# Optimization experiments

Measured on AMD Instinct MI355X. Metric: run time of the kernel, lower is better.

Reference implementation:

```python
import jax, jax.numpy as jnp
import numpy as np
from jax import lax

K_ITERS = 35

def _conv3x3_same(x, w, b):
    # x: [B,1,H,W], w: [1,1,3,3]
    y = lax.conv_general_dilated(x, w, window_strides=(1, 1),
                                 padding=((1, 1), (1, 1)),
                                 dimension_numbers=('NCHW', 'OIHW', 'NCHW'))
    return y + b.reshape(1, -1, 1, 1)

def _maxpool3x3_same(v):
    # 3x3 max pool, stride 1, padding 1 (torch MaxPool2d(kernel=3, stride=1, padding=1))
    return lax.reduce_window(v, -jnp.inf, lax.max,
                             window_dimensions=(1, 1, 3, 3),
                             window_strides=(1, 1, 1, 1),
                             padding=((0, 0), (0, 0), (1, 1), (1, 1)))

def setup_inputs() -> dict:
    key = jax.random.key(0)
    k1, k2, k3 = jax.random.split(key, 3)
    B, H, W = 64, 192, 192
    X = jax.random.uniform(k1, (B, 2, H, W), dtype=jnp.float32)  # grid, goal in [0,1)
    hp_w = jax.random.uniform(k2, (1, 1, 3, 3), dtype=jnp.float32) * 0.5
    p_w = jax.random.uniform(k3, (1, 1, 3, 3), dtype=jnp.float32) * 0.5
    hp_b = jnp.zeros((1,), dtype=jnp.float32)
    p_b = jnp.zeros((1,), dtype=jnp.float32)
    return {"X": X, "hp_w": hp_w, "hp_b": hp_b, "p_w": p_w, "p_b": p_b}

def reference(X, hp_w, hp_b, p_w, p_b):
    grid = X[:, 0:1]           # [B,1,H,W]
    goal = X[:, 1:2]           # [B,1,H,W]
    r = -(1.0 - goal)          # reward map in [-1, 0]
    # process_image: double conv -> wall/flow probability p in (0,1)
    h = jax.nn.relu(_conv3x3_same(grid, hp_w, hp_b))
    p = jax.nn.sigmoid(_conv3x3_same(h, p_w, p_b))
    # value iteration: v = max(v, r + p * (maxpool(v) - r)), k=35 steps
    def body(_, v):
        return jnp.maximum(v, r + p * (_maxpool3x3_same(v) - r))
    v = lax.fori_loop(0, K_ITERS, body, r)
    return (v[:, 0], p[:, 0])  # squeeze channel dim -> ([B,H,W], [B,H,W])
```

## Files before the change

kernel.cpp:

```cpp
#include <hip/hip_runtime.h>

#define HH 192
#define WW 192
#define HW 36864
#define BB 64
#define NPIX 2359296
#define NEG (-1.0e30f)

__global__ __launch_bounds__(256) void k_conv_fused(const float* __restrict__ X,
                                                    const float* __restrict__ hw9,
                                                    const float* __restrict__ hb,
                                                    const float* __restrict__ pw9,
                                                    const float* __restrict__ pb,
                                                    float* __restrict__ p_out) {
  int idx = blockIdx.x * 256 + threadIdx.x;
  if (idx >= NPIX / 4) return;
  int b = idx / (HW / 4);
  int rem = idx - b * (HW / 4);
  int y = rem / 48;
  int ch = rem - y * 48;
  int x0 = ch * 4;
  const float* g = X + (size_t)b * (2 * HW);

  float gr[5][8];
#pragma unroll
  for (int ry = 0; ry < 5; ++ry) {
    int yy = y - 2 + ry;
    if (yy < 0 || yy >= HH) {
#pragma unroll
      for (int j = 0; j < 8; ++j) gr[ry][j] = 0.f;
    } else {
      const float* row = g + yy * WW;
      float4 a = (x0 >= 4) ? *(const float4*)(row + x0 - 4) : make_float4(0, 0, 0, 0);
      float4 m = *(const float4*)(row + x0);
      float4 cq = (x0 + 4 < WW) ? *(const float4*)(row + x0 + 4) : make_float4(0, 0, 0, 0);
      gr[ry][0] = a.z; gr[ry][1] = a.w;
      gr[ry][2] = m.x; gr[ry][3] = m.y; gr[ry][4] = m.z; gr[ry][5] = m.w;
      gr[ry][6] = cq.x; gr[ry][7] = cq.y;
    }
  }
  float hwv[9], pwv[9];
#pragma unroll
  for (int i = 0; i < 9; ++i) { hwv[i] = hw9[i]; pwv[i] = pw9[i]; }
  float hbv = hb[0], pbv = pb[0];

  float hr[3][6];
#pragma unroll
  for (int ry = 0; ry < 3; ++ry) {
    int yy = y - 1 + ry;
    bool rowok = (yy >= 0 && yy < HH);
#pragma unroll
    for (int j = 0; j < 6; ++j) {
      int xx = x0 - 1 + j;
      float acc = hbv;
#pragma unroll
      for (int di = 0; di < 3; ++di)
#pragma unroll
        for (int dj = 0; dj < 3; ++dj)
          acc = fmaf(gr[ry + di][j + dj], hwv[di * 3 + dj], acc);
      hr[ry][j] = (rowok && xx >= 0 && xx < WW) ? fmaxf(acc, 0.f) : 0.f;
    }
  }
  float o[4];
#pragma unroll
  for (int k = 0; k < 4; ++k) {
    float acc = pbv;
#pragma unroll
    for (int di = 0; di < 3; ++di)
#pragma unroll
      for (int dj = 0; dj < 3; ++dj)
        acc = fmaf(hr[di][k + dj], pwv[di * 3 + dj], acc);
    o[k] = 1.f / (1.f + __expf(-acc));
  }
  *(float4*)(p_out + (size_t)b * HW + y * WW + x0) = make_float4(o[0], o[1], o[2], o[3]);
}

template <int FIRST>
__global__ __launch_bounds__(256, 1) void k_span(const float* __restrict__ v_in,
                                                 const float* __restrict__ p_glob,
                                                 const float* __restrict__ X,
                                                 float* __restrict__ v_out) {
  int wid = blockIdx.x * 4 + (threadIdx.x >> 6);
  int lane = threadIdx.x & 63;
  int b = wid >> 4;
  int t = wid & 15;
  int ti = t >> 2, tj = t & 3;
  int ly = lane >> 3, lx = lane & 7;
  int py = ti * 48 - 8 + ly * 8;
  int px = tj * 48 - 8 + lx * 8;
  bool colok = (px >= 0 && px < WW);

  const float* gimg = X + (size_t)b * (2 * HW) + HW;
  const float* pimg = p_glob + (size_t)b * HW;
  const float* vimg = v_in + (size_t)b * HW;

  float v[8][8], p[8][8], c[8][8];

#pragma unroll
  for (int r = 0; r < 8; ++r) {
    int gy = py + r;
    if (colok && gy >= 0 && gy < HH) {
      *(float4*)&p[r][0] = *(const float4*)(pimg + gy * WW + px);
      *(float4*)&p[r][4] = *(const float4*)(pimg + gy * WW + px + 4);
    }
  }
#pragma unroll
  for (int r = 0; r < 8; ++r) {
    int gy = py + r;
    if (colok && gy >= 0 && gy < HH) {
      *(float4*)&c[r][0] = *(const float4*)(gimg + gy * WW + px);
      *(float4*)&c[r][4] = *(const float4*)(gimg + gy * WW + px + 4);
    }
  }
  if (!FIRST) {
#pragma unroll
    for (int r = 0; r < 8; ++r) {
      int gy = py + r;
      if (colok && gy >= 0 && gy < HH) {
        *(float4*)&v[r][0] = *(const float4*)(vimg + gy * WW + px);
        *(float4*)&v[r][4] = *(const float4*)(vimg + gy * WW + px + 4);
      }
    }
  }

#pragma unroll
  for (int r = 0; r < 8; ++r) {
    int gy = py + r;
    if (colok && gy >= 0 && gy < HH) {
#pragma unroll
      for (int j = 0; j < 8; ++j) {
        float gg = c[r][j];
        if (FIRST) v[r][j] = gg - 1.f;
        c[r][j] = (gg - 1.f) * (1.f - p[r][j]);
      }
    } else {
#pragma unroll
      for (int j = 0; j < 8; ++j) { v[r][j] = NEG; p[r][j] = 0.f; c[r][j] = NEG; }
    }
  }

  int lup = (lane - 8) & 63, ldn = (lane + 8) & 63;
  int llt = (lane - 1) & 63, lrt = (lane + 1) & 63;

#pragma unroll 1
  for (int it = 0; it < 7; ++it) {
    float th[8], bh[8];
#pragma unroll
    for (int j = 0; j < 8; ++j) { float s = __shfl(v[7][j], lup, 64); th[j] = (ly == 0) ? NEG : s; }
#pragma unroll
    for (int j = 0; j < 8; ++j) { float s = __shfl(v[0][j], ldn, 64); bh[j] = (ly == 7) ? NEG : s; }
    float vm[8][8];
#pragma unroll
    for (int r = 0; r < 8; ++r) {
#pragma unroll
      for (int j = 0; j < 8; ++j) {
        float up = (r == 0) ? th[j] : v[r - 1][j];
        float dn = (r == 7) ? bh[j] : v[r + 1][j];
        vm[r][j] = fmaxf(fmaxf(up, dn), v[r][j]);
      }
    }
#pragma unroll
    for (int r = 0; r < 8; ++r) {
      float sl = __shfl(vm[r][7], llt, 64);
      float sr = __shfl(vm[r][0], lrt, 64);
      float lvm = (lx == 0) ? NEG : sl;
      float rvm = (lx == 7) ? NEG : sr;
      float hm0 = fmaxf(lvm, fmaxf(vm[r][0], vm[r][1]));
      float hm7 = fmaxf(vm[r][6], fmaxf(vm[r][7], rvm));
      v[r][0] = fmaxf(v[r][0], fmaf(p[r][0], hm0, c[r][0]));
#pragma unroll
      for (int j = 1; j < 7; ++j) {
        float hm = fmaxf(vm[r][j - 1], fmaxf(vm[r][j], vm[r][j + 1]));
        v[r][j] = fmaxf(v[r][j], fmaf(p[r][j], hm, c[r][j]));
      }
      v[r][7] = fmaxf(v[r][7], fmaf(p[r][7], hm7, c[r][7]));
    }
  }

  if (ly >= 1 && ly <= 6 && lx >= 1 && lx <= 6) {
    float* wimg = v_out + (size_t)b * HW;
#pragma unroll
    for (int r = 0; r < 8; ++r) {
      *(float4*)(wimg + (py + r) * WW + px) = make_float4(v[r][0], v[r][1], v[r][2], v[r][3]);
      *(float4*)(wimg + (py + r) * WW + px + 4) = make_float4(v[r][4], v[r][5], v[r][6], v[r][7]);
    }
  }
}

extern "C" void kernel_launch(void* const* d_in, const int* in_sizes, int n_in,
                              void* d_out, int out_size, void* d_ws, size_t ws_size,
                              hipStream_t stream) {
  const float* X = (const float*)d_in[0];
  const float* hp_w = (const float*)d_in[1];
  const float* hp_b = (const float*)d_in[2];
  const float* p_w = (const float*)d_in[3];
  const float* p_b = (const float*)d_in[4];

  float* out = (float*)d_out;
  float* out_v = out;
  float* out_p = out + NPIX;
  float* bufA = (float*)d_ws;

  int nblk = (NPIX / 4 + 255) / 256;
  k_conv_fused<<<nblk, 256, 0, stream>>>(X, hp_w, hp_b, p_w, p_b, out_p);

  k_span<1><<<256, 256, 0, stream>>>(X , out_p, X, out_v);
  k_span<0><<<256, 256, 0, stream>>>(out_v, out_p, X, bufA);
  k_span<0><<<256, 256, 0, stream>>>(bufA, out_p, X, out_v);
  k_span<0><<<256, 256, 0, stream>>>(out_v, out_p, X, bufA);
  k_span<0><<<256, 256, 0, stream>>>(bufA, out_p, X, out_v);
}
```

Before: 160.8 us.

## Fuse five value-iteration span kernels into one cooperative kernel with grid sync

Replaces the five separate span launches with a single cooperative kernel. It keeps p, c and v in registers across spans and uses grid.sync between spans, so only the halo lanes reload v from global memory after each span. This is meant to remove four launch gaps and the repeated global loads of p, goal and v. In exchange it adds grid barrier cost and needs a second workspace buffer, and it falls back to the old launches if the cooperative launch fails.

```diff
diff --git a/kernel.cpp b/kernel.cpp
--- a/kernel.cpp
+++ b/kernel.cpp
@@ -1,9 +1,10 @@
 #include <hip/hip_runtime.h>
+#include <hip/hip_cooperative_groups.h>
+namespace cg = cooperative_groups;
 
 #define HH 192
 #define WW 192
 #define HW 36864
-#define BB 64
 #define NPIX 2359296
 #define NEG (-1.0e30f)
 
@@ -75,6 +76,129 @@
   *(float4*)(p_out + (size_t)b * HW + y * WW + x0) = make_float4(o[0], o[1], o[2], o[3]);
 }
 
+__device__ __forceinline__ void iter7(float v[8][8], const float p[8][8], const float c[8][8],
+                                      int ly, int lx, int lup, int ldn, int llt, int lrt) {
+#pragma unroll 1
+  for (int it = 0; it < 7; ++it) {
+    float th[8], bh[8];
+#pragma unroll
+    for (int j = 0; j < 8; ++j) { float s = __shfl(v[7][j], lup, 64); th[j] = (ly == 0) ? NEG : s; }
+#pragma unroll
+    for (int j = 0; j < 8; ++j) { float s = __shfl(v[0][j], ldn, 64); bh[j] = (ly == 7) ? NEG : s; }
+    float vm[8][8];
+#pragma unroll
+    for (int r = 0; r < 8; ++r) {
+#pragma unroll
+      for (int j = 0; j < 8; ++j) {
+        float up = (r == 0) ? th[j] : v[r - 1][j];
+        float dn = (r == 7) ? bh[j] : v[r + 1][j];
+        vm[r][j] = fmaxf(fmaxf(up, dn), v[r][j]);
+      }
+    }
+#pragma unroll
+    for (int r = 0; r < 8; ++r) {
+      float sl = __shfl(vm[r][7], llt, 64);
+      float sr = __shfl(vm[r][0], lrt, 64);
+      float lvm = (lx == 0) ? NEG : sl;
+      float rvm = (lx == 7) ? NEG : sr;
+      float hm0 = fmaxf(lvm, fmaxf(vm[r][0], vm[r][1]));
+      float hm7 = fmaxf(vm[r][6], fmaxf(vm[r][7], rvm));
+      v[r][0] = fmaxf(v[r][0], fmaf(p[r][0], hm0, c[r][0]));
+#pragma unroll
+      for (int j = 1; j < 7; ++j) {
+        float hm = fmaxf(vm[r][j - 1], fmaxf(vm[r][j], vm[r][j + 1]));
+        v[r][j] = fmaxf(v[r][j], fmaf(p[r][j], hm, c[r][j]));
+      }
+      v[r][7] = fmaxf(v[r][7], fmaf(p[r][7], hm7, c[r][7]));
+    }
+  }
+}
+
+__global__ __launch_bounds__(256, 1) void k_vi(const float* __restrict__ p_glob,
+                                               const float* __restrict__ X,
+                                               float* __restrict__ out_v,
+                                               float* __restrict__ bufA,
+                                               float* __restrict__ bufB) {
+  cg::grid_group grid = cg::this_grid();
+  int wid = blockIdx.x * 4 + (threadIdx.x >> 6);
+  int lane = threadIdx.x & 63;
+  int b = wid >> 4;
+  int t = wid & 15;
+  int ti = t >> 2, tj = t & 3;
+  int ly = lane >> 3, lx = lane & 7;
+  int py = ti * 48 - 8 + ly * 8;
+  int px = tj * 48 - 8 + lx * 8;
+  bool colok = (px >= 0 && px < WW);
+
+  const float* gimg = X + (size_t)b * (2 * HW) + HW;
+  const float* pimg = p_glob + (size_t)b * HW;
+
+  float v[8][8], p[8][8], c[8][8];
+#pragma unroll
+  for (int r = 0; r < 8; ++r) {
+    int gy = py + r;
+    if (colok && gy >= 0 && gy < HH) {
+      *(float4*)&p[r][0] = *(const float4*)(pimg + gy * WW + px);
+      *(float4*)&p[r][4] = *(const float4*)(pimg + gy * WW + px + 4);
+    }
+  }
+#pragma unroll
+  for (int r = 0; r < 8; ++r) {
+    int gy = py + r;
+    if (colok && gy >= 0 && gy < HH) {
+      *(float4*)&c[r][0] = *(const float4*)(gimg + gy * WW + px);
+      *(float4*)&c[r][4] = *(const float4*)(gimg + gy * WW + px + 4);
+    }
+  }
+#pragma unroll
+  for (int r = 0; r < 8; ++r) {
+    int gy = py + r;
+    if (colok && gy >= 0 && gy < HH) {
+#pragma unroll
+      for (int j = 0; j < 8; ++j) {
+        float gg = c[r][j];
+        v[r][j] = gg - 1.f;
+        c[r][j] = (gg - 1.f) * (1.f - p[r][j]);
+      }
+    } else {
+#pragma unroll
+      for (int j = 0; j < 8; ++j) { v[r][j] = NEG; p[r][j] = 0.f; c[r][j] = NEG; }
+    }
+  }
+
+  int lup = (lane - 8) & 63, ldn = (lane + 8) & 63;
+  int llt = (lane - 1) & 63, lrt = (lane + 1) & 63;
+
+  for (int span = 0; span < 5; ++span) {
+    iter7(v, p, c, ly, lx, lup, ldn, llt, lrt);
+
+    float* wb = (span == 4) ? out_v : ((span & 1) ? bufB : bufA);
+    float* wimg = wb + (size_t)b * HW;
+    if (ly >= 1 && ly <= 6 && lx >= 1 && lx <= 6) {
+#pragma unroll
+      for (int r = 0; r < 8; ++r) {
+        *(float4*)(wimg + (py + r) * WW + px) = make_float4(v[r][0], v[r][1], v[r][2], v[r][3]);
+        *(float4*)(wimg + (py + r) * WW + px + 4) = make_float4(v[r][4], v[r][5], v[r][6], v[r][7]);
+      }
+    }
+    if (span < 4) {
+      grid.sync();
+      if (ly == 0 || ly == 7 || lx == 0 || lx == 7) {
+#pragma unroll
+        for (int r = 0; r < 8; ++r) {
+          int gy = py + r;
+          if (colok && gy >= 0 && gy < HH) {
+            float4 a = *(const float4*)(wimg + gy * WW + px);
+            float4 d = *(const float4*)(wimg + gy * WW + px + 4);
+            v[r][0] = a.x; v[r][1] = a.y; v[r][2] = a.z; v[r][3] = a.w;
+            v[r][4] = d.x; v[r][5] = d.y; v[r][6] = d.z; v[r][7] = d.w;
+          }
+        }
+      }
+    }
+  }
+}
+
 template <int FIRST>
 __global__ __launch_bounds__(256, 1) void k_span(const float* __restrict__ v_in,
                                                  const float* __restrict__ p_glob,
@@ -95,7 +219,6 @@
   const float* vimg = v_in + (size_t)b * HW;
 
   float v[8][8], p[8][8], c[8][8];
-
 #pragma unroll
   for (int r = 0; r < 8; ++r) {
     int gy = py + r;
@@ -122,7 +245,6 @@
       }
     }
   }
-
 #pragma unroll
   for (int r = 0; r < 8; ++r) {
     int gy = py + r;
@@ -142,40 +264,7 @@
   int lup = (lane - 8) & 63, ldn = (lane + 8) & 63;
   int llt = (lane - 1) & 63, lrt = (lane + 1) & 63;
 
-#pragma unroll 1
-  for (int it = 0; it < 7; ++it) {
-    float th[8], bh[8];
-#pragma unroll
-    for (int j = 0; j < 8; ++j) { float s = __shfl(v[7][j], lup, 64); th[j] = (ly == 0) ? NEG : s; }
-#pragma unroll
-    for (int j = 0; j < 8; ++j) { float s = __shfl(v[0][j], ldn, 64); bh[j] = (ly == 7) ? NEG : s; }
-    float vm[8][8];
-#pragma unroll
-    for (int r = 0; r < 8; ++r) {
-#pragma unroll
-      for (int j = 0; j < 8; ++j) {
-        float up = (r == 0) ? th[j] : v[r - 1][j];
-        float dn = (r == 7) ? bh[j] : v[r + 1][j];
-        vm[r][j] = fmaxf(fmaxf(up, dn), v[r][j]);
-      }
-    }
-#pragma unroll
-    for (int r = 0; r < 8; ++r) {
-      float sl = __shfl(vm[r][7], llt, 64);
-      float sr = __shfl(vm[r][0], lrt, 64);
-      float lvm = (lx == 0) ? NEG : sl;
-      float rvm = (lx == 7) ? NEG : sr;
-      float hm0 = fmaxf(lvm, fmaxf(vm[r][0], vm[r][1]));
-      float hm7 = fmaxf(vm[r][6], fmaxf(vm[r][7], rvm));
-      v[r][0] = fmaxf(v[r][0], fmaf(p[r][0], hm0, c[r][0]));
-#pragma unroll
-      for (int j = 1; j < 7; ++j) {
-        float hm = fmaxf(vm[r][j - 1], fmaxf(vm[r][j], vm[r][j + 1]));
-        v[r][j] = fmaxf(v[r][j], fmaf(p[r][j], hm, c[r][j]));
-      }
-      v[r][7] = fmaxf(v[r][7], fmaf(p[r][7], hm7, c[r][7]));
-    }
-  }
+  iter7(v, p, c, ly, lx, lup, ldn, llt, lrt);
 
   if (ly >= 1 && ly <= 6 && lx >= 1 && lx <= 6) {
     float* wimg = v_out + (size_t)b * HW;
@@ -200,13 +289,21 @@
   float* out_v = out;
   float* out_p = out + NPIX;
   float* bufA = (float*)d_ws;
+  float* bufB = bufA + NPIX;
 
   int nblk = (NPIX / 4 + 255) / 256;
   k_conv_fused<<<nblk, 256, 0, stream>>>(X, hp_w, hp_b, p_w, p_b, out_p);
 
-  k_span<1><<<256, 256, 0, stream>>>(X , out_p, X, out_v);
-  k_span<0><<<256, 256, 0, stream>>>(out_v, out_p, X, bufA);
-  k_span<0><<<256, 256, 0, stream>>>(bufA, out_p, X, out_v);
-  k_span<0><<<256, 256, 0, stream>>>(out_v, out_p, X, bufA);
-  k_span<0><<<256, 256, 0, stream>>>(bufA, out_p, X, out_v);
-}
+  const float* p_c = out_p;
+  void* args[] = { (void*)&p_c, (void*)&X, (void*)&out_v, (void*)&bufA, (void*)&bufB };
+  hipError_t e = hipLaunchCooperativeKernel((const void*)k_vi, dim3(256), dim3(256),
+                                            args, 0, stream);
+  if (e != hipSuccess) {
+    (void)hipGetLastError();
+    k_span<1><<<256, 256, 0, stream>>>(X , out_p, X, out_v);
+    k_span<0><<<256, 256, 0, stream>>>(out_v, out_p, X, bufA);
+    k_span<0><<<256, 256, 0, stream>>>(bufA, out_p, X, out_v);
+    k_span<0><<<256, 256, 0, stream>>>(out_v, out_p, X, bufA);
+    k_span<0><<<256, 256, 0, stream>>>(bufA, out_p, X, out_v);
+  }
+}
```

Result: slower. 292.8 us (+82.1%).

## Fuse five value-iteration span kernels into one cooperative kernel with grid sync

Applied to the files above, without the earlier changes.

Replaces the five k_span launches with a single cooperative kernel, k_vi, that keeps v, p and c in registers across all spans. Between spans it writes interior results to a ping-pong buffer, calls grid.sync(), and reloads only the halo lanes from global memory. This removes four kernel launches and the repeated reloads of p, goal and v per span. In exchange it relies on cooperative launch support (256 blocks at one block per CU must be co-resident) and pays for grid-wide barriers; if the cooperative launch fails it falls back to the old kernels. It also needs a second workspace buffer.

```diff
diff --git a/kernel.cpp b/kernel.cpp
--- a/kernel.cpp
+++ b/kernel.cpp
@@ -1,9 +1,10 @@
 #include <hip/hip_runtime.h>
+#include <hip/hip_cooperative_groups.h>
+namespace cg = cooperative_groups;
 
 #define HH 192
 #define WW 192
 #define HW 36864
-#define BB 64
 #define NPIX 2359296
 #define NEG (-1.0e30f)
 
@@ -75,6 +76,122 @@
   *(float4*)(p_out + (size_t)b * HW + y * WW + x0) = make_float4(o[0], o[1], o[2], o[3]);
 }
 
+#define ITER7_BODY                                                                   \
+  _Pragma("unroll 1")                                                                \
+  for (int it = 0; it < 7; ++it) {                                                   \
+    float th[8], bh[8];                                                              \
+    _Pragma("unroll")                                                                \
+    for (int j = 0; j < 8; ++j) { float s = __shfl(v[7][j], lup, 64); th[j] = (ly == 0) ? NEG : s; } \
+    _Pragma("unroll")                                                                \
+    for (int j = 0; j < 8; ++j) { float s = __shfl(v[0][j], ldn, 64); bh[j] = (ly == 7) ? NEG : s; } \
+    float vm[8][8];                                                                  \
+    _Pragma("unroll")                                                                \
+    for (int r = 0; r < 8; ++r) {                                                    \
+      _Pragma("unroll")                                                              \
+      for (int j = 0; j < 8; ++j) {                                                  \
+        float up = (r == 0) ? th[j] : v[r - 1][j];                                   \
+        float dn = (r == 7) ? bh[j] : v[r + 1][j];                                   \
+        vm[r][j] = fmaxf(fmaxf(up, dn), v[r][j]);                                    \
+      }                                                                              \
+    }                                                                                \
+    _Pragma("unroll")                                                                \
+    for (int r = 0; r < 8; ++r) {                                                    \
+      float sl = __shfl(vm[r][7], llt, 64);                                          \
+      float sr = __shfl(vm[r][0], lrt, 64);                                          \
+      float lvm = (lx == 0) ? NEG : sl;                                              \
+      float rvm = (lx == 7) ? NEG : sr;                                              \
+      float hm0 = fmaxf(lvm, fmaxf(vm[r][0], vm[r][1]));                             \
+      float hm7 = fmaxf(vm[r][6], fmaxf(vm[r][7], rvm));                             \
+      v[r][0] = fmaxf(v[r][0], fmaf(p[r][0], hm0, c[r][0]));                         \
+      _Pragma("unroll")                                                              \
+      for (int j = 1; j < 7; ++j) {                                                  \
+        float hm = fmaxf(vm[r][j - 1], fmaxf(vm[r][j], vm[r][j + 1]));               \
+        v[r][j] = fmaxf(v[r][j], fmaf(p[r][j], hm, c[r][j]));                        \
+      }                                                                              \
+      v[r][7] = fmaxf(v[r][7], fmaf(p[r][7], hm7, c[r][7]));                         \
+    }                                                                                \
+  }
+
+#define SPREAD8(dst_row, t0, t1)                                                     \
+  dst_row[0] = t0.x; dst_row[1] = t0.y; dst_row[2] = t0.z; dst_row[3] = t0.w;        \
+  dst_row[4] = t1.x; dst_row[5] = t1.y; dst_row[6] = t1.z; dst_row[7] = t1.w;
+
+__global__ __launch_bounds__(256, 1) void k_vi(const float* __restrict__ p_glob,
+                                               const float* __restrict__ X,
+                                               float* __restrict__ out_v,
+                                               float* __restrict__ bufA,
+                                               float* __restrict__ bufB) {
+  cg::grid_group grid = cg::this_grid();
+  int wid = blockIdx.x * 4 + (threadIdx.x >> 6);
+  int lane = threadIdx.x & 63;
+  int b = wid >> 4;
+  int t = wid & 15;
+  int ti = t >> 2, tj = t & 3;
+  int ly = lane >> 3, lx = lane & 7;
+  int py = ti * 48 - 8 + ly * 8;
+  int px = tj * 48 - 8 + lx * 8;
+  bool colok = (px >= 0 && px < WW);
+
+  const float* gimg = X + (size_t)b * (2 * HW) + HW;
+  const float* pimg = p_glob + (size_t)b * HW;
+
+  float v[8][8], p[8][8], c[8][8];
+#pragma unroll
+  for (int r = 0; r < 8; ++r) {
+    int gy = py + r;
+    if (colok && gy >= 0 && gy < HH) {
+      const float* pp = pimg + gy * WW + px;
+      const float* gp = gimg + gy * WW + px;
+      float4 tp0 = *(const float4*)(pp);
+      float4 tp1 = *(const float4*)(pp + 4);
+      float4 tg0 = *(const float4*)(gp);
+      float4 tg1 = *(const float4*)(gp + 4);
+      SPREAD8(p[r], tp0, tp1);
+      float gg[8];
+      SPREAD8(gg, tg0, tg1);
+#pragma unroll
+      for (int j = 0; j < 8; ++j) {
+        v[r][j] = gg[j] - 1.f;
+        c[r][j] = (gg[j] - 1.f) * (1.f - p[r][j]);
+      }
+    } else {
+#pragma unroll
+      for (int j = 0; j < 8; ++j) { v[r][j] = NEG; p[r][j] = 0.f; c[r][j] = NEG; }
+    }
+  }
+
+  int lup = (lane - 8) & 63, ldn = (lane + 8) & 63;
+  int llt = (lane - 1) & 63, lrt = (lane + 1) & 63;
+
+  for (int span = 0; span < 5; ++span) {
+    ITER7_BODY
+
+    float* wb = (span == 4) ? out_v : ((span & 1) ? bufB : bufA);
+    float* wimg = wb + (size_t)b * HW;
+    if (ly >= 1 && ly <= 6 && lx >= 1 && lx <= 6) {
+#pragma unroll
+      for (int r = 0; r < 8; ++r) {
+        *(float4*)(wimg + (py + r) * WW + px) = make_float4(v[r][0], v[r][1], v[r][2], v[r][3]);
+        *(float4*)(wimg + (py + r) * WW + px + 4) = make_float4(v[r][4], v[r][5], v[r][6], v[r][7]);
+      }
+    }
+    if (span < 4) {
+      grid.sync();
+      if (ly == 0 || ly == 7 || lx == 0 || lx == 7) {
+#pragma unroll
+        for (int r = 0; r < 8; ++r) {
+          int gy = py + r;
+          if (colok && gy >= 0 && gy < HH) {
+            float4 a = *(const float4*)(wimg + gy * WW + px);
+            float4 d = *(const float4*)(wimg + gy * WW + px + 4);
+            SPREAD8(v[r], a, d);
+          }
+        }
+      }
+    }
+  }
+}
+
 template <int FIRST>
 __global__ __launch_bounds__(256, 1) void k_span(const float* __restrict__ v_in,
                                                  const float* __restrict__ p_glob,
@@ -95,44 +212,31 @@
   const float* vimg = v_in + (size_t)b * HW;
 
   float v[8][8], p[8][8], c[8][8];
-
 #pragma unroll
   for (int r = 0; r < 8; ++r) {
     int gy = py + r;
     if (colok && gy >= 0 && gy < HH) {
-      *(float4*)&p[r][0] = *(const float4*)(pimg + gy * WW + px);
-      *(float4*)&p[r][4] = *(const float4*)(pimg + gy * WW + px + 4);
-    }
-  }
-#pragma unroll
-  for (int r = 0; r < 8; ++r) {
-    int gy = py + r;
-    if (colok && gy >= 0 && gy < HH) {
-      *(float4*)&c[r][0] = *(const float4*)(gimg + gy * WW + px);
-      *(float4*)&c[r][4] = *(const float4*)(gimg + gy * WW + px + 4);
-    }
-  }
-  if (!FIRST) {
-#pragma unroll
-    for (int r = 0; r < 8; ++r) {
-      int gy = py + r;
-      if (colok && gy >= 0 && gy < HH) {
-        *(float4*)&v[r][0] = *(const float4*)(vimg + gy * WW + px);
-        *(float4*)&v[r][4] = *(const float4*)(vimg + gy * WW + px + 4);
-      }
-    }
-  }
-
-#pragma unroll
-  for (int r = 0; r < 8; ++r) {
-    int gy = py + r;
-    if (colok && gy >= 0 && gy < HH) {
-#pragma unroll
-      for (int j = 0; j < 8; ++j) {
-        float gg = c[r][j];
-        if (FIRST) v[r][j] = gg - 1.f;
-        c[r][j] = (gg - 1.f) * (1.f - p[r][j]);
-      }
+      const float* pp = pimg + gy * WW + px;
+      const float* gp = gimg + gy * WW + px;
+      float4 tp0 = *(const float4*)(pp);
+      float4 tp1 = *(const float4*)(pp + 4);
+      float4 tg0 = *(const float4*)(gp);
+      float4 tg1 = *(const float4*)(gp + 4);
+      SPREAD8(p[r], tp0, tp1);
+      float gg[8];
+      SPREAD8(gg, tg0, tg1);
+      if (FIRST) {
+#pragma unroll
+        for (int j = 0; j < 8; ++j) v[r][j] = gg[j] - 1.f;
+      } else {
+        const float* vp = vimg + gy * WW + px;
+        float4 tv0 = *(const float4*)(vp);
+        float4 tv1 = *(const float4*)(vp + 4);
+        SPREAD8(v[r], tv0, tv1);
+      }
+#pragma unroll
+      for (int j = 0; j < 8; ++j)
+        c[r][j] = (gg[j] - 1.f) * (1.f - p[r][j]);
     } else {
 #pragma unroll
       for (int j = 0; j < 8; ++j) { v[r][j] = NEG; p[r][j] = 0.f; c[r][j] = NEG; }
@@ -142,40 +246,7 @@
   int lup = (lane - 8) & 63, ldn = (lane + 8) & 63;
   int llt = (lane - 1) & 63, lrt = (lane + 1) & 63;
 
-#pragma unroll 1
-  for (int it = 0; it < 7; ++it) {
-    float th[8], bh[8];
-#pragma unroll
-    for (int j = 0; j < 8; ++j) { float s = __shfl(v[7][j], lup, 64); th[j] = (ly == 0) ? NEG : s; }
-#pragma unroll
-    for (int j = 0; j < 8; ++j) { float s = __shfl(v[0][j], ldn, 64); bh[j] = (ly == 7) ? NEG : s; }
-    float vm[8][8];
-#pragma unroll
-    for (int r = 0; r < 8; ++r) {
-#pragma unroll
-      for (int j = 0; j < 8; ++j) {
-        float up = (r == 0) ? th[j] : v[r - 1][j];
-        float dn = (r == 7) ? bh[j] : v[r + 1][j];
-        vm[r][j] = fmaxf(fmaxf(up, dn), v[r][j]);
-      }
-    }
-#pragma unroll
-    for (int r = 0; r < 8; ++r) {
-      float sl = __shfl(vm[r][7], llt, 64);
-      float sr = __shfl(vm[r][0], lrt, 64);
-      float lvm = (lx == 0) ? NEG : sl;
-      float rvm = (lx == 7) ? NEG : sr;
-      float hm0 = fmaxf(lvm, fmaxf(vm[r][0], vm[r][1]));
-      float hm7 = fmaxf(vm[r][6], fmaxf(vm[r][7], rvm));
-      v[r][0] = fmaxf(v[r][0], fmaf(p[r][0], hm0, c[r][0]));
-#pragma unroll
-      for (int j = 1; j < 7; ++j) {
-        float hm = fmaxf(vm[r][j - 1], fmaxf(vm[r][j], vm[r][j + 1]));
-        v[r][j] = fmaxf(v[r][j], fmaf(p[r][j], hm, c[r][j]));
-      }
-      v[r][7] = fmaxf(v[r][7], fmaf(p[r][7], hm7, c[r][7]));
-    }
-  }
+  ITER7_BODY
 
   if (ly >= 1 && ly <= 6 && lx >= 1 && lx <= 6) {
     float* wimg = v_out + (size_t)b * HW;
@@ -200,13 +271,21 @@
   float* out_v = out;
   float* out_p = out + NPIX;
   float* bufA = (float*)d_ws;
+  float* bufB = bufA + NPIX;
 
   int nblk = (NPIX / 4 + 255) / 256;
   k_conv_fused<<<nblk, 256, 0, stream>>>(X, hp_w, hp_b, p_w, p_b, out_p);
 
-  k_span<1><<<256, 256, 0, stream>>>(X , out_p, X, out_v);
-  k_span<0><<<256, 256, 0, stream>>>(out_v, out_p, X, bufA);
-  k_span<0><<<256, 256, 0, stream>>>(bufA, out_p, X, out_v);
-  k_span<0><<<256, 256, 0, stream>>>(out_v, out_p, X, bufA);
-  k_span<0><<<256, 256, 0, stream>>>(bufA, out_p, X, out_v);
-}
+  const float* p_c = out_p;
+  void* args[] = { (void*)&p_c, (void*)&X, (void*)&out_v, (void*)&bufA, (void*)&bufB };
+  hipError_t e = hipLaunchCooperativeKernel((const void*)k_vi, dim3(256), dim3(256),
+                                            args, 0, stream);
+  if (e != hipSuccess) {
+    (void)hipGetLastError();
+    k_span<1><<<256, 256, 0, stream>>>(X , out_p, X, out_v);
+    k_span<0><<<256, 256, 0, stream>>>(out_v, out_p, X, bufA);
+    k_span<0><<<256, 256, 0, stream>>>(bufA, out_p, X, out_v);
+    k_span<0><<<256, 256, 0, stream>>>(out_v, out_p, X, bufA);
+    k_span<0><<<256, 256, 0, stream>>>(bufA, out_p, X, out_v);
+  }
+}
```

Measured after the change: 294.6 us. 1.83x slower.
